# Performance work log

Hardware: AMD Instinct MI355X
Metric: run time of the kernel (lower is better)

The kernel has to match this reference:

```python
import jax, jax.numpy as jnp
import numpy as np

BS, N_NODES, T = 64, 1024, 1200


def _conv1d(h, w, b, stride, pad):
    # h: (N, 1, L), w: (1, 1, k) -> Conv1d(1,1,k,stride,pad) + bias
    y = jax.lax.conv_general_dilated(h, w, (stride,), [(pad, pad)],
                                     dimension_numbers=("NCH", "OIH", "NCH"))
    return y + b[None, :, None]


def _maxpool1d(h, k):
    # kernel=k, stride=k (PyTorch default stride=None -> kernel_size), VALID
    return jax.lax.reduce_window(h, -jnp.inf, jax.lax.max, (1, 1, k), (1, 1, k), "VALID")


def _gcn_ones_adj(h, W, b, n):
    # GCNConv with A = ones(n,n): A_hat = A + I, deg = n+1 uniformly,
    agg = (h + h.sum(axis=1, keepdims=True)) / (n + 1.0)
    return jnp.einsum("bnf,fg->bng", agg, W) + b


def setup_inputs() -> dict:
    key = jax.random.key(0)
    ks = jax.random.split(key, 16)
    p = lambda k, shp: jax.random.normal(k, shp, dtype=jnp.float32) * 0.1
    return {
        "x": jax.random.normal(ks[0], (BS, N_NODES, T), dtype=jnp.float32),
        "c0_w": p(ks[1], (1, 1, 2)), "c0_b": p(ks[2], (1,)),
        "c2_w": p(ks[3], (1, 1, 4)), "c2_b": p(ks[4], (1,)),
        "c4_w": p(ks[5], (1, 1, 4)), "c4_b": p(ks[6], (1,)),
        "c6_w": p(ks[7], (1, 1, 4)), "c6_b": p(ks[8], (1,)),
        "c8_w": p(ks[9], (1, 1, 3)), "c8_b": p(ks[10], (1,)),
        "gcn1_w": p(ks[11], (50, 50)), "gcn1_b": p(ks[12], (50,)),
        "gcn2_w": p(ks[13], (12, 12)), "gcn2_b": p(ks[14], (12,)),
        "cls_w": p(ks[15], (3, N_NODES)),
        "cls_b": jnp.zeros((3,), dtype=jnp.float32),
    }


def reference(x, c0_w, c0_b, c2_w, c2_b, c4_w, c4_b, c6_w, c6_b, c8_w, c8_b,
              gcn1_w, gcn1_b, gcn2_w, gcn2_b, cls_w, cls_b):
    bs, n, t = x.shape
    h = x.reshape(bs * n, 1, t)                 # batch all nodes together
    h = _conv1d(h, c0_w, c0_b, 2, 0)            # i=0: L=600
    h = jax.nn.relu(_maxpool1d(h, 3))           # i=1: L=200
    h = _conv1d(h, c2_w, c2_b, 2, 1)            # i=2: L=100
    h = jax.nn.relu(_maxpool1d(h, 2))           # i=3: L=50
    # i==4: source applies gcn1 to t_layer_out[4] AFTER it was consumed -> dead code
    _ = _gcn_ones_adj(h.reshape(bs, n, -1), gcn1_w, gcn1_b, n)
    h = _conv1d(h, c4_w, c4_b, 2, 1)            # i=4: L=25
    h = jax.nn.relu(_maxpool1d(h, 2))           # i=5: L=12
    # i==6: same dead-code pattern for gcn2
    _ = _gcn_ones_adj(h.reshape(bs, n, -1), gcn2_w, gcn2_b, n)
    h = _conv1d(h, c6_w, c6_b, 2, 1)            # i=6: L=6
    h = jax.nn.relu(_maxpool1d(h, 2))           # i=7: L=3
    h = _conv1d(h, c8_w, c8_b, 1, 0)            # i=8: L=1
    feat = h.reshape(bs, n)                     # (bs, n_nodes)
    logits = feat @ cls_w.T + cls_b
    return jax.nn.softmax(logits, axis=1)
```

## Files before the change

kernel.cpp:

```cpp
#include <hip/hip_runtime.h>
#include <math.h>

#define BS 64
#define NN 1024
#define T  1200
#define NSEQ (BS * NN)


__global__ __launch_bounds__(256) void chain_kernel(
    const float* __restrict__ x,
    const float* __restrict__ c0_w, const float* __restrict__ c0_b,
    const float* __restrict__ c2_w, const float* __restrict__ c2_b,
    const float* __restrict__ c4_w, const float* __restrict__ c4_b,
    const float* __restrict__ c6_w, const float* __restrict__ c6_b,
    const float* __restrict__ c8_w, const float* __restrict__ c8_b,
    float* __restrict__ feat)
{
    __shared__ __align__(16) float smem[4][2000];
    const int wave = threadIdx.x >> 6;
    const int lane = threadIdx.x & 63;
    const int seq  = blockIdx.x * 4 + wave;

    float* sx = smem[wave];
    float* sA = sx + 1200;
    float* sB = sx + 1800;

    const float w00 = c0_w[0], w01 = c0_w[1], b0 = c0_b[0];
    const float w20 = c2_w[0], w21 = c2_w[1], w22 = c2_w[2], w23 = c2_w[3], b2 = c2_b[0];
    const float w40 = c4_w[0], w41 = c4_w[1], w42 = c4_w[2], w43 = c4_w[3], b4 = c4_b[0];
    const float w60 = c6_w[0], w61 = c6_w[1], w62 = c6_w[2], w63 = c6_w[3], b6 = c6_b[0];
    const float w80 = c8_w[0], w81 = c8_w[1], w82 = c8_w[2], b8 = c8_b[0];

    const float4* xg = (const float4*)(x + (size_t)seq * T);
    float4* sx4 = (float4*)sx;
    for (int i = lane; i < 300; i += 64) {
        sx4[i] = xg[i];
    }
    __syncthreads();

    for (int j = lane; j < 600; j += 64) {
        sA[j] = w00 * sx[2*j] + w01 * sx[2*j + 1] + b0;
    }
    __syncthreads();

    for (int p = lane; p < 200; p += 64) {
        float m = fmaxf(sA[3*p], fmaxf(sA[3*p + 1], sA[3*p + 2]));
        sB[p] = fmaxf(m, 0.0f);
    }
    __syncthreads();

    for (int j = lane; j < 100; j += 64) {
        int base = 2*j - 1;
        float acc = b2;
        float v0 = (base + 0 >= 0   ) ? sB[base + 0] : 0.0f;
        float v3 = (base + 3 <  200 ) ? sB[base + 3] : 0.0f;
        acc += w20 * v0 + w21 * sB[base + 1] + w22 * sB[base + 2] + w23 * v3;
        sA[j] = acc;
    }
    __syncthreads();

    for (int p = lane; p < 50; p += 64) {
        sB[p] = fmaxf(fmaxf(sA[2*p], sA[2*p + 1]), 0.0f);
    }
    __syncthreads();

    for (int j = lane; j < 25; j += 64) {
        int base = 2*j - 1;
        float acc = b4;
        float v0 = (base + 0 >= 0 ) ? sB[base + 0] : 0.0f;
        float v3 = (base + 3 < 50 ) ? sB[base + 3] : 0.0f;
        acc += w40 * v0 + w41 * sB[base + 1] + w42 * sB[base + 2] + w43 * v3;
        sA[j] = acc;
    }
    __syncthreads();

    for (int p = lane; p < 12; p += 64) {
        sB[p] = fmaxf(fmaxf(sA[2*p], sA[2*p + 1]), 0.0f);
    }
    __syncthreads();

    for (int j = lane; j < 6; j += 64) {
        int base = 2*j - 1;
        float acc = b6;
        float v0 = (base + 0 >= 0 ) ? sB[base + 0] : 0.0f;
        float v3 = (base + 3 < 12 ) ? sB[base + 3] : 0.0f;
        acc += w60 * v0 + w61 * sB[base + 1] + w62 * sB[base + 2] + w63 * v3;
        sA[j] = acc;
    }
    __syncthreads();

    for (int p = lane; p < 3; p += 64) {
        sB[p] = fmaxf(fmaxf(sA[2*p], sA[2*p + 1]), 0.0f);
    }
    __syncthreads();

    if (lane == 0) {
        feat[seq] = w80 * sB[0] + w81 * sB[1] + w82 * sB[2] + b8;
    }
}

__global__ __launch_bounds__(256) void head_kernel(
    const float* __restrict__ feat,
    const float* __restrict__ cls_w,
    const float* __restrict__ cls_b,
    float* __restrict__ out)
{
    const int b = blockIdx.x;
    float a0 = 0.0f, a1 = 0.0f, a2 = 0.0f;
    for (int n = threadIdx.x; n < NN; n += 256) {
        float f = feat[b * NN + n];
        a0 += f * cls_w[0 * NN + n];
        a1 += f * cls_w[1 * NN + n];
        a2 += f * cls_w[2 * NN + n];
    }
    for (int off = 32; off; off >>= 1) {
        a0 += __shfl_down(a0, off);
        a1 += __shfl_down(a1, off);
        a2 += __shfl_down(a2, off);
    }
    __shared__ float red[4][3];
    const int wave = threadIdx.x >> 6;
    const int lane = threadIdx.x & 63;
    if (lane == 0) { red[wave][0] = a0; red[wave][1] = a1; red[wave][2] = a2; }
    __syncthreads();
    if (threadIdx.x == 0) {
        float l0 = red[0][0] + red[1][0] + red[2][0] + red[3][0] + cls_b[0];
        float l1 = red[0][1] + red[1][1] + red[2][1] + red[3][1] + cls_b[1];
        float l2 = red[0][2] + red[1][2] + red[2][2] + red[3][2] + cls_b[2];
        float m  = fmaxf(l0, fmaxf(l1, l2));
        float e0 = expf(l0 - m), e1 = expf(l1 - m), e2 = expf(l2 - m);
        float inv = 1.0f / (e0 + e1 + e2);
        out[b * 3 + 0] = e0 * inv;
        out[b * 3 + 1] = e1 * inv;
        out[b * 3 + 2] = e2 * inv;
    }
}

extern "C" void kernel_launch(void* const* d_in, const int* in_sizes, int n_in,
                              void* d_out, int out_size, void* d_ws, size_t ws_size,
                              hipStream_t stream) {
    const float* x     = (const float*)d_in[0];
    const float* c0_w  = (const float*)d_in[1];
    const float* c0_b  = (const float*)d_in[2];
    const float* c2_w  = (const float*)d_in[3];
    const float* c2_b  = (const float*)d_in[4];
    const float* c4_w  = (const float*)d_in[5];
    const float* c4_b  = (const float*)d_in[6];
    const float* c6_w  = (const float*)d_in[7];
    const float* c6_b  = (const float*)d_in[8];
    const float* c8_w  = (const float*)d_in[9];
    const float* c8_b  = (const float*)d_in[10];
    const float* cls_w = (const float*)d_in[15];
    const float* cls_b = (const float*)d_in[16];

    float* feat = (float*)d_ws;

    chain_kernel<<<NSEQ / 4, 256, 0, stream>>>(
        x, c0_w, c0_b, c2_w, c2_b, c4_w, c4_b, c6_w, c6_b, c8_w, c8_b, feat);
    head_kernel<<<BS, 256, 0, stream>>>(feat, cls_w, cls_b, (float*)d_out);
}
```

Measured before the change: 442.8 us.

## Fuse conv/maxpool stage pairs and replace block barriers with wave-local LDS waits

Each conv and its following maxpool are now computed in one pass, so intermediates are never stored and the number of LDS round trips drops. The global load is unrolled into five float4 loads per lane, and the shared-memory footprint per wave shrinks. __syncthreads is replaced by an s_waitcnt lgkmcnt(0) wave-level wait, since each wave works on its own sequence. The tail stages run in registers on lane 0. The risk is that relying on in-wave LDS ordering without a barrier is correct only while each sequence stays within one 64-wide wave.

```diff
diff --git a/kernel.cpp b/kernel.cpp
--- a/kernel.cpp
+++ b/kernel.cpp
@@ -5,6 +5,8 @@
 #define NN 1024
 #define T  1200
 #define NSEQ (BS * NN)
+
+#define WAVE_SYNC() asm volatile("s_waitcnt lgkmcnt(0)" ::: "memory")
 
 
 __global__ __launch_bounds__(256) void chain_kernel(
@@ -16,14 +18,13 @@
     const float* __restrict__ c8_w, const float* __restrict__ c8_b,
     float* __restrict__ feat)
 {
-    __shared__ __align__(16) float smem[4][2000];
+    __shared__ __align__(16) float smem[4][1400];
     const int wave = threadIdx.x >> 6;
     const int lane = threadIdx.x & 63;
     const int seq  = blockIdx.x * 4 + wave;
 
     float* sx = smem[wave];
-    float* sA = sx + 1200;
-    float* sB = sx + 1800;
+    float* sB = sx + 1200;
 
     const float w00 = c0_w[0], w01 = c0_w[1], b0 = c0_b[0];
     const float w20 = c2_w[0], w21 = c2_w[1], w22 = c2_w[2], w23 = c2_w[3], b2 = c2_b[0];
@@ -31,71 +32,82 @@
     const float w60 = c6_w[0], w61 = c6_w[1], w62 = c6_w[2], w63 = c6_w[3], b6 = c6_b[0];
     const float w80 = c8_w[0], w81 = c8_w[1], w82 = c8_w[2], b8 = c8_b[0];
 
-    const float4* xg = (const float4*)(x + (size_t)seq * T);
+    const float4* xg4 = (const float4*)(x + (size_t)seq * T);
     float4* sx4 = (float4*)sx;
-    for (int i = lane; i < 300; i += 64) {
-        sx4[i] = xg[i];
+    float4 r0 = xg4[lane];
+    float4 r1 = xg4[lane + 64];
+    float4 r2 = xg4[lane + 128];
+    float4 r3 = xg4[lane + 192];
+    const bool tail = lane < 44;
+    float4 r4 = make_float4(0.f, 0.f, 0.f, 0.f);
+    if (tail) r4 = xg4[lane + 256];
+    sx4[lane]       = r0;
+    sx4[lane + 64]  = r1;
+    sx4[lane + 128] = r2;
+    sx4[lane + 192] = r3;
+    if (tail) sx4[lane + 256] = r4;
+    WAVE_SYNC();
+
+#pragma unroll
+    for (int it = 0; it < 4; ++it) {
+        int p = lane + it * 64;
+        if (p < 200) {
+            const float* xp = sx + 6 * p;
+            float x0 = xp[0], x1 = xp[1], x2 = xp[2], x3 = xp[3], x4 = xp[4], x5 = xp[5];
+            float c0 = fmaf(w00, x0, fmaf(w01, x1, b0));
+            float c1 = fmaf(w00, x2, fmaf(w01, x3, b0));
+            float c2 = fmaf(w00, x4, fmaf(w01, x5, b0));
+            sB[p] = fmaxf(fmaxf(fmaxf(c0, c1), c2), 0.0f);
+        }
     }
-    __syncthreads();
+    WAVE_SYNC();
 
-    for (int j = lane; j < 600; j += 64) {
-        sA[j] = w00 * sx[2*j] + w01 * sx[2*j + 1] + b0;
+    if (lane < 50) {
+        int base = 4 * lane - 1;
+        float v0 = sB[base < 0 ? 0 : base];
+        float v1 = sB[base + 1];
+        float v2 = sB[base + 2];
+        float v3 = sB[base + 3];
+        float v4 = sB[base + 4];
+        float v5 = sB[(base + 5) > 199 ? 199 : (base + 5)];
+        if (lane == 0)  v0 = 0.0f;
+        if (lane == 49) v5 = 0.0f;
+        float oa = fmaf(w20, v0, fmaf(w21, v1, fmaf(w22, v2, fmaf(w23, v3, b2))));
+        float ob = fmaf(w20, v2, fmaf(w21, v3, fmaf(w22, v4, fmaf(w23, v5, b2))));
+        sx[lane] = fmaxf(fmaxf(oa, ob), 0.0f);
     }
-    __syncthreads();
+    WAVE_SYNC();
 
-    for (int p = lane; p < 200; p += 64) {
-        float m = fmaxf(sA[3*p], fmaxf(sA[3*p + 1], sA[3*p + 2]));
-        sB[p] = fmaxf(m, 0.0f);
+    if (lane < 12) {
+        int base = 4 * lane - 1;
+        float u0 = sx[base < 0 ? 0 : base];
+        float u1 = sx[base + 1];
+        float u2 = sx[base + 2];
+        float u3 = sx[base + 3];
+        float u4 = sx[base + 4];
+        float u5 = sx[base + 5];
+        if (lane == 0) u0 = 0.0f;
+        float oa = fmaf(w40, u0, fmaf(w41, u1, fmaf(w42, u2, fmaf(w43, u3, b4))));
+        float ob = fmaf(w40, u2, fmaf(w41, u3, fmaf(w42, u4, fmaf(w43, u5, b4))));
+        sx[64 + lane] = fmaxf(fmaxf(oa, ob), 0.0f);
     }
-    __syncthreads();
-
-    for (int j = lane; j < 100; j += 64) {
-        int base = 2*j - 1;
-        float acc = b2;
-        float v0 = (base + 0 >= 0   ) ? sB[base + 0] : 0.0f;
-        float v3 = (base + 3 <  200 ) ? sB[base + 3] : 0.0f;
-        acc += w20 * v0 + w21 * sB[base + 1] + w22 * sB[base + 2] + w23 * v3;
-        sA[j] = acc;
-    }
-    __syncthreads();
-
-    for (int p = lane; p < 50; p += 64) {
-        sB[p] = fmaxf(fmaxf(sA[2*p], sA[2*p + 1]), 0.0f);
-    }
-    __syncthreads();
-
-    for (int j = lane; j < 25; j += 64) {
-        int base = 2*j - 1;
-        float acc = b4;
-        float v0 = (base + 0 >= 0 ) ? sB[base + 0] : 0.0f;
-        float v3 = (base + 3 < 50 ) ? sB[base + 3] : 0.0f;
-        acc += w40 * v0 + w41 * sB[base + 1] + w42 * sB[base + 2] + w43 * v3;
-        sA[j] = acc;
-    }
-    __syncthreads();
-
-    for (int p = lane; p < 12; p += 64) {
-        sB[p] = fmaxf(fmaxf(sA[2*p], sA[2*p + 1]), 0.0f);
-    }
-    __syncthreads();
-
-    for (int j = lane; j < 6; j += 64) {
-        int base = 2*j - 1;
-        float acc = b6;
-        float v0 = (base + 0 >= 0 ) ? sB[base + 0] : 0.0f;
-        float v3 = (base + 3 < 12 ) ? sB[base + 3] : 0.0f;
-        acc += w60 * v0 + w61 * sB[base + 1] + w62 * sB[base + 2] + w63 * v3;
-        sA[j] = acc;
-    }
-    __syncthreads();
-
-    for (int p = lane; p < 3; p += 64) {
-        sB[p] = fmaxf(fmaxf(sA[2*p], sA[2*p + 1]), 0.0f);
-    }
-    __syncthreads();
+    WAVE_SYNC();
 
     if (lane == 0) {
-        feat[seq] = w80 * sB[0] + w81 * sB[1] + w82 * sB[2] + b8;
+        float a3[14];
+        a3[0] = 0.0f; a3[13] = 0.0f;
+#pragma unroll
+        for (int j = 0; j < 12; ++j) a3[j + 1] = sx[64 + j];
+        float o[6];
+#pragma unroll
+        for (int j = 0; j < 6; ++j) {
+            o[j] = fmaf(w60, a3[2 * j], fmaf(w61, a3[2 * j + 1],
+                   fmaf(w62, a3[2 * j + 2], fmaf(w63, a3[2 * j + 3], b6))));
+        }
+        float A40 = fmaxf(fmaxf(o[0], o[1]), 0.0f);
+        float A41 = fmaxf(fmaxf(o[2], o[3]), 0.0f);
+        float A42 = fmaxf(fmaxf(o[4], o[5]), 0.0f);
+        feat[seq] = fmaf(w80, A40, fmaf(w81, A41, fmaf(w82, A42, b8)));
     }
 }
 
```

After: 438.1 us. About the same (-1.1%).
